# Kernel optimization log

Hardware: AMD Instinct MI355X
Metric: run time of the kernel (lower is better)

The kernel has to match this reference:

```python
import jax, jax.numpy as jnp
import numpy as np

B, S, D = 32, 512, 512
GH, LH = 8, 4            # global / local num_heads
W, STRIDE = 10, 5        # local window size and hop (window_size // 2)


def _mha(x, w_in, b_in, w_out, b_out, n_heads, key_mask=None):
    """Torch nn.MultiheadAttention (self-attn, eval mode). x: [N, L, D]."""
    N, L, d = x.shape
    dh = d // n_heads
    qkv = x @ w_in.T + b_in                       # [N, L, 3D]
    q, k, v = jnp.split(qkv, 3, axis=-1)
    def heads(t):
        return t.reshape(N, L, n_heads, dh).transpose(0, 2, 1, 3)  # [N,H,L,dh]
    q, k, v = heads(q), heads(k), heads(v)
    scores = jnp.einsum('bhqd,bhkd->bhqk', q, k) / jnp.sqrt(jnp.asarray(dh, x.dtype))
    if key_mask is not None:                      # key_mask: [N, L] bool, True = valid
        scores = jnp.where(key_mask[:, None, None, :], scores, jnp.asarray(-1e9, x.dtype))
    attn = jax.nn.softmax(scores, axis=-1)
    out = jnp.einsum('bhqk,bhkd->bhqd', attn, v).transpose(0, 2, 1, 3).reshape(N, L, d)
    return out @ w_out.T + b_out


def setup_inputs() -> dict:
    key = jax.random.key(0)
    ks = jax.random.split(key, 12)
    s = 0.02
    return {
        'x':      jax.random.normal(ks[0], (B, S, D), jnp.float32),
        'gw_in':  jax.random.normal(ks[1], (3 * D, D), jnp.float32) * s,
        'gb_in':  jnp.zeros((3 * D,), jnp.float32),
        'gw_out': jax.random.normal(ks[2], (D, D), jnp.float32) * s,
        'gb_out': jnp.zeros((D,), jnp.float32),
        'lw_in':  jax.random.normal(ks[3], (3 * D, D), jnp.float32) * s,
        'lb_in':  jnp.zeros((3 * D,), jnp.float32),
        'lw_out': jax.random.normal(ks[4], (D, D), jnp.float32) * s,
        'lb_out': jnp.zeros((D,), jnp.float32),
        'fw':     jax.random.normal(ks[5], (D, 2 * D), jnp.float32) * s,
        'fb':     jnp.zeros((D,), jnp.float32),
    }


def reference(x, gw_in, gb_in, gw_out, gb_out, lw_in, lb_in, lw_out, lb_out, fw, fb):
    # ---- global branch: full self-attention over the sequence ----
    global_out = _mha(x, gw_in, gb_in, gw_out, gb_out, GH)

    # ---- local branch: overlapping windows of size W, hop STRIDE ----
    starts = np.arange(0, S, STRIDE)              # static window starts
    NW = len(starts)
    pos = starts[:, None] + np.arange(W)          # [NW, W] absolute positions
    valid = pos < S                               # ragged tail windows
    idx = np.minimum(pos, S - 1)                  # clipped gather indices

    windows = x[:, idx]                           # [B, NW, W, D]
    windows = windows.reshape(B * NW, W, D)
    key_mask = jnp.broadcast_to(jnp.asarray(valid)[None], (B, NW, W)).reshape(B * NW, W)

    local_attn = _mha(windows, lw_in, lb_in, lw_out, lb_out, LH, key_mask=key_mask)
    local_attn = local_attn.reshape(B, NW, W, D) * jnp.asarray(valid)[None, :, :, None].astype(x.dtype)

    # scatter-add overlapping window outputs back (matches `local_out[:, i:end] +=`)
    local_out = jnp.zeros_like(x).at[:, idx.reshape(-1)].add(local_attn.reshape(B, NW * W, D))

    # ---- fusion MLP (dropout = identity in eval) ----
    combined = jnp.concatenate([global_out, local_out], axis=-1)   # [B, S, 2D]
    return jax.nn.relu(combined @ fw.T + fb)
```

## Files before the change

### kernel.cpp

```cpp
#include <hip/hip_runtime.h>
#include <cstdint>
#include <cstddef>

#define DEV __device__ __forceinline__

typedef float f32x4 __attribute__((ext_vector_type(4)));
typedef short bf16x8 __attribute__((ext_vector_type(8)));

DEV unsigned short f2bf(float f) {
  union { float f; unsigned u; } v; v.f = f;
  unsigned u = v.u;
  unsigned r = u + 0x7FFFu + ((u >> 16) & 1u);
  return (unsigned short)(r >> 16);
}
DEV float bf2f(unsigned short h) {
  union { unsigned u; float f; } v; v.u = ((unsigned)h) << 16;
  return v.f;
}
DEV unsigned cvtpk(float lo, float hi) {
  unsigned r;
  asm("v_cvt_pk_bf16_f32 %0, %1, %2" : "=v"(r) : "v"(lo), "v"(hi));
  return r;
}

DEV void gload16(const void* g, void* l) {
  __builtin_amdgcn_global_load_lds((const __attribute__((address_space(1))) unsigned int*)g,
                                   (__attribute__((address_space(3))) unsigned int*)l,
                                   16, 0, 0);
}

DEV f32x4 MFMA(bf16x8 a, bf16x8 b, f32x4 c) {
  return __builtin_amdgcn_mfma_f32_16x16x32_bf16(a, b, c, 0, 0, 0);
}

__global__ void k_f2bf(const float* __restrict__ src, unsigned short* __restrict__ dst, int n) {
  int i = (blockIdx.x * blockDim.x + threadIdx.x) * 4;
  int stride = gridDim.x * blockDim.x * 4;
  for (; i < n; i += stride) {
    float4 v = *(const float4*)(src + i);
    ushort4 o;
    o.x = f2bf(v.x); o.y = f2bf(v.y); o.z = f2bf(v.z); o.w = f2bf(v.w);
    *(ushort4*)(dst + i) = o;
  }
}

__global__ __launch_bounds__(256) void k_merge(const float* __restrict__ fw,
                                               const float* __restrict__ gw_out,
                                               const float* __restrict__ lw_out,
                                               unsigned short* __restrict__ M1b,
                                               unsigned short* __restrict__ M2b) {
  __shared__ float Fa[64][68];
  __shared__ float Gb[64][68];
  const int bi = blockIdx.x, bj = blockIdx.y, m2 = blockIdx.z;
  const float* g = m2 ? lw_out : gw_out;
  const int i0 = bi * 64, j0 = bj * 64;
  const int tid = threadIdx.x;
  const int tr = tid >> 4, tc = tid & 15;
  float acc[4][4] = {};
  for (int kc = 0; kc < 8; kc++) {
    int k0 = kc * 64;
    __syncthreads();
    #pragma unroll
    for (int it = 0; it < 4; it++) {
      int r = tr + 16 * it;
      float4 v = *(const float4*)(fw + (size_t)(i0 + r) * 1024 + m2 * 512 + k0 + tc * 4);
      Fa[tc * 4 + 0][r] = v.x; Fa[tc * 4 + 1][r] = v.y;
      Fa[tc * 4 + 2][r] = v.z; Fa[tc * 4 + 3][r] = v.w;
      *(float4*)&Gb[r][tc * 4] = *(const float4*)(g + (size_t)(k0 + r) * 512 + j0 + tc * 4);
    }
    __syncthreads();
    for (int k = 0; k < 64; k++) {
      float4 a4 = *(const float4*)&Fa[k][tr * 4];
      float4 b4 = *(const float4*)&Gb[k][tc * 4];
      float av[4] = {a4.x, a4.y, a4.z, a4.w};
      float bv[4] = {b4.x, b4.y, b4.z, b4.w};
      #pragma unroll
      for (int r = 0; r < 4; r++)
        #pragma unroll
        for (int c = 0; c < 4; c++)
          acc[r][c] += av[r] * bv[c];
    }
  }
  unsigned short* M = m2 ? M2b : M1b;
  #pragma unroll
  for (int r = 0; r < 4; r++) {
    ushort4 pk;
    pk.x = f2bf(acc[r][0]); pk.y = f2bf(acc[r][1]);
    pk.z = f2bf(acc[r][2]); pk.w = f2bf(acc[r][3]);
    *(ushort4*)&M[(size_t)(i0 + tr * 4 + r) * 512 + j0 + tc * 4] = pk;
  }
}

__global__ __launch_bounds__(256) void k_bias(const float* __restrict__ fw, const float* __restrict__ gb_out,
                                              const float* __restrict__ lb_out, const float* __restrict__ fb,
                                              float* __restrict__ bias1, float* __restrict__ bias2) {
  __shared__ float bv[512];
  const int which = blockIdx.y;
  const int i0 = blockIdx.x * 64;
  const float* src = which ? lb_out : gb_out;
  for (int t = threadIdx.x; t < 512; t += 256) bv[t] = src[t];
  __syncthreads();
  const int r = threadIdx.x >> 2, c4 = threadIdx.x & 3;
  const float* frow = fw + (size_t)(i0 + r) * 1024 + (which ? 512 : 0) + c4 * 128;
  float a = 0.f;
  #pragma unroll 4
  for (int k = 0; k < 128; k += 4) {
    float4 v = *(const float4*)(frow + k);
    a += v.x * bv[c4 * 128 + k] + v.y * bv[c4 * 128 + k + 1]
       + v.z * bv[c4 * 128 + k + 2] + v.w * bv[c4 * 128 + k + 3];
  }
  a += __shfl_xor(a, 1);
  a += __shfl_xor(a, 2);
  if (c4 == 0) {
    int i = i0 + r;
    if (which) bias2[i] = a;
    else       bias1[i] = a + fb[i];
  }
}

template <int EPI>
__global__ __launch_bounds__(256) void k_gemm(const unsigned short* __restrict__ A,
                                              const unsigned short* __restrict__ A2,
                                              const unsigned short* __restrict__ Wm,
                                              const unsigned short* __restrict__ W2,
                                              const float* __restrict__ bias,
                                              const float* __restrict__ bias2,
                                              float qscale, void* __restrict__ Cout,
                                              int Ntot, int NT) {
  __shared__ unsigned short As[2][128 * 32];
  __shared__ unsigned short Bs[2][128 * 32];
  const int tid = threadIdx.x;
  const int wave = tid >> 6, lane = tid & 63;
  const int wr = wave >> 1, wc = wave & 1;
  const int bm = blockIdx.x, bn = blockIdx.y;
  const int ql = lane & 15, kg = lane >> 4;

  const int c0 = wave * 2;
  const int srow = lane >> 2;
  const int sks = (lane & 3) * 8;

  auto stage = [&](int buf, int t) {
    const unsigned short* sA = A;
    const unsigned short* sW = Wm;
    int k0 = t * 32;
    if (EPI == 1 && t >= 16) { sA = A2; sW = W2; k0 = (t - 16) * 32; }
    #pragma unroll
    for (int i = 0; i < 2; i++) {
      int c = c0 + i;
      int row = c * 16 + srow;
      gload16(sA + (size_t)(bm * 128 + row) * 512 + k0 + sks, &As[buf][c * 512 + lane * 8]);
      gload16(sW + (size_t)(bn * 128 + row) * 512 + k0 + sks, &Bs[buf][c * 512 + lane * 8]);
    }
  };

  f32x4 acc[4][4] = {};
  stage(0, 0);
  __syncthreads();
  for (int t = 0; t < NT; t++) {
    int buf = t & 1;
    if (t + 1 < NT) stage(buf ^ 1, t + 1);
    const unsigned short* as = As[buf];
    const unsigned short* bs = Bs[buf];
    bf16x8 af[4], bfr[4];
    #pragma unroll
    for (int m = 0; m < 4; m++)
      af[m] = *(const bf16x8*)&as[(wr * 64 + m * 16 + ql) * 32 + kg * 8];
    #pragma unroll
    for (int n = 0; n < 4; n++)
      bfr[n] = *(const bf16x8*)&bs[(wc * 64 + n * 16 + ql) * 32 + kg * 8];
    #pragma unroll
    for (int m = 0; m < 4; m++)
      #pragma unroll
      for (int n = 0; n < 4; n++)
        acc[m][n] = MFMA(af[m], bfr[n], acc[m][n]);
    __syncthreads();
  }

  const int row0 = bm * 128 + wr * 64;
  const int col0 = bn * 128 + wc * 64;
  if (EPI == 0) {
    unsigned short* C = (unsigned short*)Cout;
    #pragma unroll
    for (int m = 0; m < 4; m++)
      #pragma unroll
      for (int n = 0; n < 4; n++) {
        int col = col0 + n * 16 + ql;
        float bcol = bias[col];
        float qs = (col < 512) ? qscale : 1.0f;
        #pragma unroll
        for (int r = 0; r < 4; r++) {
          int row = row0 + m * 16 + kg * 4 + r;
          C[(size_t)row * Ntot + col] = f2bf((acc[m][n][r] + bcol) * qs);
        }
      }
  } else {
    float* C = (float*)Cout;
    #pragma unroll
    for (int m = 0; m < 4; m++)
      #pragma unroll
      for (int n = 0; n < 4; n++) {
        int col = col0 + n * 16 + ql;
        float b1 = bias[col], b2 = bias2[col];
        #pragma unroll
        for (int r = 0; r < 4; r++) {
          int row = row0 + m * 16 + kg * 4 + r;
          float cc = ((row & 511) < 5) ? 1.0f : 2.0f;
          float v = acc[m][n][r] + b1 + cc * b2;
          C[(size_t)row * 512 + col] = fmaxf(v, 0.0f);
        }
      }
  }
}

__global__ __launch_bounds__(1024, 4) void k_attn_g(const unsigned short* __restrict__ QKV,
                                                    unsigned short* __restrict__ Og) {
  __shared__ unsigned short Klds[512 * 64];
  __shared__ unsigned short Vt[64 * 512];
  const int tid = threadIdx.x, wave = tid >> 6, lane = tid & 63;
  const int ql = lane & 15, kg = lane >> 4;
  const int h = blockIdx.x, b = blockIdx.y;
  const size_t tb = (size_t)b * 512;
  const size_t hoff = (size_t)h * 64;

  #pragma unroll
  for (int i = 0; i < 4; i++) {
    int instr = wave * 4 + i;
    int row = instr * 8 + (lane >> 3);
    int slot = lane & 7;
    int c = slot ^ (row & 7);
    gload16(QKV + (tb + row) * 1536 + 512 + hoff + c * 8, &Klds[instr * 512 + lane * 8]);
  }
  {
    int key = tid & 511;
    int cb = (tid >> 9) * 4;
    int k64 = key & 63;
    int f = k64 >> 4, kgv = (k64 >> 2) & 3, r = k64 & 3;
    int col = (key & ~63) + 32 * (f >> 1) + 4 * (f & 1) + 8 * kgv + r;
    const unsigned short* Vp = QKV + (tb + key) * 1536 + 1024 + hoff;
    #pragma unroll
    for (int c8 = 0; c8 < 4; c8++) {
      bf16x8 v8 = *(const bf16x8*)(Vp + (cb + c8) * 8);
      #pragma unroll
      for (int j = 0; j < 8; j++) {
        int d = (cb + c8) * 8 + j;
        Vt[d * 512 + (((col >> 3) ^ (d & 7)) * 8) + (col & 7)] = (unsigned short)v8[j];
      }
    }
  }
  bf16x8 qf[2][2];
  #pragma unroll
  for (int m = 0; m < 2; m++) {
    const unsigned short* Qp = QKV + (tb + wave * 32 + m * 16 + ql) * 1536 + hoff;
    qf[m][0] = *(const bf16x8*)(Qp + kg * 8);
    qf[m][1] = *(const bf16x8*)(Qp + 32 + kg * 8);
  }
  __syncthreads();

  float l_part[2] = {};
  f32x4 ot[2][4] = {};

  for (int kv = 0; kv < 8; kv++) {
    const int k0 = kv * 64;
    bf16x8 kf[4][2], vb[4][2];
    #pragma unroll
    for (int f = 0; f < 4; f++) {
      int row = k0 + 16 * f + ql;
      #pragma unroll
      for (int c = 0; c < 2; c++)
        kf[f][c] = *(const bf16x8*)&Klds[row * 64 + (((c * 4 + kg) ^ (row & 7)) * 8)];
      int d = 16 * f + ql;
      #pragma unroll
      for (int st = 0; st < 2; st++) {
        int cb_r = (k0 >> 3) + st * 4 + kg;
        vb[f][st] = *(const bf16x8*)&Vt[d * 512 + ((cb_r ^ (d & 7)) * 8)];
      }
    }
    #pragma unroll
    for (int m = 0; m < 2; m++) {
      f32x4 s[4] = {};
      #pragma unroll
      for (int f = 0; f < 4; f++) {
        s[f] = MFMA(kf[f][0], qf[m][0], s[f]);
        s[f] = MFMA(kf[f][1], qf[m][1], s[f]);
      }
      #pragma unroll
      for (int f = 0; f < 4; f++) {
        #pragma unroll
        for (int r = 0; r < 4; r++)
          s[f][r] = exp2f(s[f][r]);
        l_part[m] += (s[f][0] + s[f][1]) + (s[f][2] + s[f][3]);
      }
      #pragma unroll
      for (int st = 0; st < 2; st++) {
        union { unsigned w[4]; bf16x8 v; } pb;
        #pragma unroll
        for (int w = 0; w < 4; w++) {
          int f = 2 * st + (w >> 1);
          pb.w[w] = cvtpk(s[f][2 * (w & 1)], s[f][2 * (w & 1) + 1]);
        }
        #pragma unroll
        for (int fp = 0; fp < 4; fp++)
          ot[m][fp] = MFMA(vb[fp][st], pb.v, ot[m][fp]);
      }
    }
  }

  #pragma unroll
  for (int m = 0; m < 2; m++) {
    float l = l_part[m];
    l += __shfl_xor(l, 16);
    l += __shfl_xor(l, 32);
    float inv = 1.0f / l;
    size_t row = tb + wave * 32 + m * 16 + ql;
    #pragma unroll
    for (int fp = 0; fp < 4; fp++) {
      ushort4 st4;
      st4.x = f2bf(ot[m][fp][0] * inv);
      st4.y = f2bf(ot[m][fp][1] * inv);
      st4.z = f2bf(ot[m][fp][2] * inv);
      st4.w = f2bf(ot[m][fp][3] * inv);
      *(ushort4*)&Og[row * 512 + hoff + 16 * fp + 4 * kg] = st4;
    }
  }
}

__global__ __launch_bounds__(256) void k_attn_l(const unsigned short* __restrict__ QKV,
                                                unsigned short* __restrict__ Lacc) {
  __shared__ unsigned short Qs[5][520];
  __shared__ unsigned short Ks[15][520];
  __shared__ unsigned short Vs[15][520];
  __shared__ float Pb[2][4][5][13];
  const int w = blockIdx.x, b = blockIdx.y;
  const int p0 = 5 * w;
  const int tid = threadIdx.x;
  const size_t tbase = (size_t)b * 512;

  for (int c = tid; c < 35 * 64; c += 256) {
    int row = c >> 6, ch = (c & 63) * 8;
    if (row < 5) {
      int tok = min(p0 + row, 511);
      *(bf16x8*)&Qs[row][ch] = *(const bf16x8*)(QKV + (tbase + tok) * 1536 + ch);
    } else if (row < 20) {
      int rr = row - 5;
      int tok = min(max(p0 - 5 + rr, 0), 511);
      *(bf16x8*)&Ks[rr][ch] = *(const bf16x8*)(QKV + (tbase + tok) * 1536 + 512 + ch);
    } else {
      int rr = row - 20;
      int tok = min(max(p0 - 5 + rr, 0), 511);
      *(bf16x8*)&Vs[rr][ch] = *(const bf16x8*)(QKV + (tbase + tok) * 1536 + 1024 + ch);
    }
  }
  __syncthreads();

  #pragma unroll
  for (int rep = 0; rep < 2; rep++) {
    int idx = tid + rep * 256;
    if (idx < 400) {
      int j = idx % 10;
      int t1 = idx / 10;
      int q = t1 % 5;
      int t2 = t1 / 5;
      int h = t2 & 3;
      int win = t2 >> 2;
      int krow = win ? j : j + 5;
      int ktok = p0 - 5 + krow;
      float scv = -1e30f;
      bool ok = (win == 0 || w > 0) && (p0 + q < 512) && (ktok < 512);
      if (ok) {
        float acc = 0.f;
        const unsigned short* qp = &Qs[q][h * 128];
        const unsigned short* kp = &Ks[krow][h * 128];
        #pragma unroll
        for (int ck = 0; ck < 16; ck++) {
          bf16x8 q8 = *(const bf16x8*)(qp + ck * 8);
          bf16x8 k8 = *(const bf16x8*)(kp + ck * 8);
          #pragma unroll
          for (int e = 0; e < 8; e++)
            acc += bf2f((unsigned short)q8[e]) * bf2f((unsigned short)k8[e]);
        }
        scv = acc;
      }
      Pb[win][h][q][j] = scv;
    }
  }
  __syncthreads();

  if (tid < 40) {
    int q = tid % 5;
    int t2 = tid / 5;
    int h = t2 & 3;
    int win = t2 >> 2;
    float* row = &Pb[win][h][q][0];
    float mx = -1e30f;
    #pragma unroll
    for (int j = 0; j < 10; j++) mx = fmaxf(mx, row[j]);
    float e[10]; float su = 0.f;
    #pragma unroll
    for (int j = 0; j < 10; j++) {
      float v = row[j];
      float ej = (v <= -1e29f) ? 0.f : exp2f(v - mx);
      e[j] = ej; su += ej;
    }
    float inv = (su > 0.f) ? 1.0f / su : 0.f;
    #pragma unroll
    for (int j = 0; j < 10; j++) row[j] = e[j] * inv;
  }
  __syncthreads();

  {
    const int h = tid >> 6;
    const int d = tid * 2;
    for (int qq = 0; qq < 5; qq++) {
      int p = p0 + qq;
      if (p >= 512) break;
      float a0 = 0.f, a1 = 0.f;
      const float* P0 = &Pb[0][h][qq][0];
      #pragma unroll
      for (int j = 0; j < 10; j++) {
        float pw = P0[j];
        a0 += pw * bf2f(Vs[j + 5][d]);
        a1 += pw * bf2f(Vs[j + 5][d + 1]);
      }
      if (w > 0) {
        const float* P1 = &Pb[1][h][qq][0];
        #pragma unroll
        for (int j = 0; j < 10; j++) {
          float pw = P1[j];
          a0 += pw * bf2f(Vs[j][d]);
          a1 += pw * bf2f(Vs[j][d + 1]);
        }
      }
      ushort2 st; st.x = f2bf(a0); st.y = f2bf(a1);
      *(ushort2*)&Lacc[(tbase + p) * 512 + d] = st;
    }
  }
}

extern "C" void kernel_launch(void* const* d_in, const int* in_sizes, int n_in,
                              void* d_out, int out_size, void* d_ws, size_t ws_size,
                              hipStream_t stream) {
  const float* x      = (const float*)d_in[0];
  const float* gw_in  = (const float*)d_in[1];
  const float* gb_in  = (const float*)d_in[2];
  const float* gw_out = (const float*)d_in[3];
  const float* gb_out = (const float*)d_in[4];
  const float* lw_in  = (const float*)d_in[5];
  const float* lb_in  = (const float*)d_in[6];
  const float* lw_out = (const float*)d_in[7];
  const float* lb_out = (const float*)d_in[8];
  const float* fw     = (const float*)d_in[9];
  const float* fb     = (const float*)d_in[10];

  char* ws = (char*)d_ws;
  auto alloc = [&](size_t bytes) -> char* {
    char* p = ws;
    ws += (bytes + 255) & ~(size_t)255;
    return p;
  };
  unsigned short* xb     = (unsigned short*)alloc((size_t)16384 * 512 * 2);
  unsigned short* gwin_b = (unsigned short*)alloc((size_t)1536 * 512 * 2);
  unsigned short* lwin_b = (unsigned short*)alloc((size_t)1536 * 512 * 2);
  unsigned short* M1b    = (unsigned short*)alloc((size_t)512 * 512 * 2);
  unsigned short* M2b    = (unsigned short*)alloc((size_t)512 * 512 * 2);
  float* bias1           = (float*)alloc(512 * 4);
  float* bias2           = (float*)alloc(512 * 4);
  unsigned short* QKV    = (unsigned short*)alloc((size_t)16384 * 1536 * 2);
  unsigned short* Og     = (unsigned short*)alloc((size_t)16384 * 512 * 2);
  unsigned short* La     = (unsigned short*)alloc((size_t)16384 * 512 * 2);

  k_f2bf<<<2048, 256, 0, stream>>>(x, xb, 16384 * 512);
  k_f2bf<<<128, 256, 0, stream>>>(gw_in, gwin_b, 1536 * 512);
  k_f2bf<<<128, 256, 0, stream>>>(lw_in, lwin_b, 1536 * 512);
  k_merge<<<dim3(8, 8, 2), 256, 0, stream>>>(fw, gw_out, lw_out, M1b, M2b);
  k_bias<<<dim3(8, 2), 256, 0, stream>>>(fw, gb_out, lb_out, fb, bias1, bias2);

  k_gemm<0><<<dim3(128, 12), 256, 0, stream>>>(xb, nullptr, gwin_b, nullptr, gb_in, nullptr,
                                               0.125f * 1.44269504f, QKV, 1536, 16);
  k_attn_g<<<dim3(8, 32), 1024, 0, stream>>>(QKV, Og);

  k_gemm<0><<<dim3(128, 12), 256, 0, stream>>>(xb, nullptr, lwin_b, nullptr, lb_in, nullptr,
                                               0.08838834764831845f * 1.44269504f, QKV, 1536, 16);
  k_attn_l<<<dim3(103, 32), 256, 0, stream>>>(QKV, La);

  k_gemm<1><<<dim3(128, 4), 256, 0, stream>>>(Og, La, M1b, M2b, bias1, bias2,
                                              1.0f, d_out, 512, 32);
}
```

Before: 214.9 us.

## Restructure GEMM to two waves with 128x64 per-wave tiles and XOR-swizzled LDS

The bf16 GEMM now runs with 128 threads (2 waves) per 128x128 block instead of 4 waves. Each wave computes a 128x64 output tile with 8x4 MFMA accumulators, so each LDS B fragment is reused across 8 A fragments. The shared-memory staging layout gains an XOR swizzle on the k-chunk index to avoid bank conflicts on fragment reads. The aim is more MFMA work per LDS read and fewer bank conflicts. The cost is double the accumulator registers per wave and fewer waves to hide memory latency.

```diff
diff --git a/kernel.cpp b/kernel.cpp
--- a/kernel.cpp
+++ b/kernel.cpp
@@ -119,25 +119,20 @@
 }
 
 template <int EPI>
-__global__ __launch_bounds__(256) void k_gemm(const unsigned short* __restrict__ A,
-                                              const unsigned short* __restrict__ A2,
-                                              const unsigned short* __restrict__ Wm,
-                                              const unsigned short* __restrict__ W2,
-                                              const float* __restrict__ bias,
-                                              const float* __restrict__ bias2,
-                                              float qscale, void* __restrict__ Cout,
-                                              int Ntot, int NT) {
+__global__ __launch_bounds__(128) void k_gemm2(const unsigned short* __restrict__ A,
+                                               const unsigned short* __restrict__ A2,
+                                               const unsigned short* __restrict__ Wm,
+                                               const unsigned short* __restrict__ W2,
+                                               const float* __restrict__ bias,
+                                               const float* __restrict__ bias2,
+                                               float qscale, void* __restrict__ Cout,
+                                               int Ntot, int NT) {
   __shared__ unsigned short As[2][128 * 32];
   __shared__ unsigned short Bs[2][128 * 32];
   const int tid = threadIdx.x;
   const int wave = tid >> 6, lane = tid & 63;
-  const int wr = wave >> 1, wc = wave & 1;
   const int bm = blockIdx.x, bn = blockIdx.y;
   const int ql = lane & 15, kg = lane >> 4;
-
-  const int c0 = wave * 2;
-  const int srow = lane >> 2;
-  const int sks = (lane & 3) * 8;
 
   auto stage = [&](int buf, int t) {
     const unsigned short* sA = A;
@@ -145,67 +140,69 @@
     int k0 = t * 32;
     if (EPI == 1 && t >= 16) { sA = A2; sW = W2; k0 = (t - 16) * 32; }
     #pragma unroll
-    for (int i = 0; i < 2; i++) {
-      int c = c0 + i;
-      int row = c * 16 + srow;
-      gload16(sA + (size_t)(bm * 128 + row) * 512 + k0 + sks, &As[buf][c * 512 + lane * 8]);
-      gload16(sW + (size_t)(bn * 128 + row) * 512 + k0 + sks, &Bs[buf][c * 512 + lane * 8]);
+    for (int i = 0; i < 4; i++) {
+      int n = i * 128 + tid;
+      int row = n >> 2, s = n & 3;
+      int c = s ^ ((row >> 1) & 3);
+      gload16(sA + (size_t)(bm * 128 + row) * 512 + k0 + c * 8, &As[buf][n * 8]);
+      gload16(sW + (size_t)(bn * 128 + row) * 512 + k0 + c * 8, &Bs[buf][n * 8]);
     }
   };
 
-  f32x4 acc[4][4] = {};
+  const int offs = ql * 32 + ((kg ^ ((ql >> 1) & 3)) * 8);
+
+  f32x4 acc[8][4] = {};
   stage(0, 0);
   __syncthreads();
   for (int t = 0; t < NT; t++) {
     int buf = t & 1;
     if (t + 1 < NT) stage(buf ^ 1, t + 1);
     const unsigned short* as = As[buf];
-    const unsigned short* bs = Bs[buf];
-    bf16x8 af[4], bfr[4];
-    #pragma unroll
-    for (int m = 0; m < 4; m++)
-      af[m] = *(const bf16x8*)&as[(wr * 64 + m * 16 + ql) * 32 + kg * 8];
-    #pragma unroll
-    for (int n = 0; n < 4; n++)
-      bfr[n] = *(const bf16x8*)&bs[(wc * 64 + n * 16 + ql) * 32 + kg * 8];
-    #pragma unroll
-    for (int m = 0; m < 4; m++)
-      #pragma unroll
-      for (int n = 0; n < 4; n++)
-        acc[m][n] = MFMA(af[m], bfr[n], acc[m][n]);
+    const unsigned short* bs = Bs[buf] + wave * 2048;
+    bf16x8 bfr[4];
+    #pragma unroll
+    for (int nq = 0; nq < 4; nq++)
+      bfr[nq] = *(const bf16x8*)(bs + nq * 512 + offs);
+    #pragma unroll
+    for (int mq = 0; mq < 8; mq++) {
+      bf16x8 af = *(const bf16x8*)(as + mq * 512 + offs);
+      #pragma unroll
+      for (int nq = 0; nq < 4; nq++)
+        acc[mq][nq] = MFMA(af, bfr[nq], acc[mq][nq]);
+    }
     __syncthreads();
   }
 
-  const int row0 = bm * 128 + wr * 64;
-  const int col0 = bn * 128 + wc * 64;
+  const int row0 = bm * 128;
+  const int col0 = bn * 128 + wave * 64;
   if (EPI == 0) {
     unsigned short* C = (unsigned short*)Cout;
     #pragma unroll
-    for (int m = 0; m < 4; m++)
-      #pragma unroll
-      for (int n = 0; n < 4; n++) {
-        int col = col0 + n * 16 + ql;
+    for (int mq = 0; mq < 8; mq++)
+      #pragma unroll
+      for (int nq = 0; nq < 4; nq++) {
+        int col = col0 + nq * 16 + ql;
         float bcol = bias[col];
         float qs = (col < 512) ? qscale : 1.0f;
         #pragma unroll
         for (int r = 0; r < 4; r++) {
-          int row = row0 + m * 16 + kg * 4 + r;
-          C[(size_t)row * Ntot + col] = f2bf((acc[m][n][r] + bcol) * qs);
+          int row = row0 + mq * 16 + kg * 4 + r;
+          C[(size_t)row * Ntot + col] = f2bf((acc[mq][nq][r] + bcol) * qs);
         }
       }
   } else {
     float* C = (float*)Cout;
     #pragma unroll
-    for (int m = 0; m < 4; m++)
-      #pragma unroll
-      for (int n = 0; n < 4; n++) {
-        int col = col0 + n * 16 + ql;
+    for (int mq = 0; mq < 8; mq++)
+      #pragma unroll
+      for (int nq = 0; nq < 4; nq++) {
+        int col = col0 + nq * 16 + ql;
         float b1 = bias[col], b2 = bias2[col];
         #pragma unroll
         for (int r = 0; r < 4; r++) {
-          int row = row0 + m * 16 + kg * 4 + r;
+          int row = row0 + mq * 16 + kg * 4 + r;
           float cc = ((row & 511) < 5) ? 1.0f : 2.0f;
-          float v = acc[m][n][r] + b1 + cc * b2;
+          float v = acc[mq][nq][r] + b1 + cc * b2;
           C[(size_t)row * 512 + col] = fmaxf(v, 0.0f);
         }
       }
@@ -474,14 +471,14 @@
   k_merge<<<dim3(8, 8, 2), 256, 0, stream>>>(fw, gw_out, lw_out, M1b, M2b);
   k_bias<<<dim3(8, 2), 256, 0, stream>>>(fw, gb_out, lb_out, fb, bias1, bias2);
 
-  k_gemm<0><<<dim3(128, 12), 256, 0, stream>>>(xb, nullptr, gwin_b, nullptr, gb_in, nullptr,
-                                               0.125f * 1.44269504f, QKV, 1536, 16);
+  k_gemm2<0><<<dim3(128, 12), 128, 0, stream>>>(xb, nullptr, gwin_b, nullptr, gb_in, nullptr,
+                                                0.125f * 1.44269504f, QKV, 1536, 16);
   k_attn_g<<<dim3(8, 32), 1024, 0, stream>>>(QKV, Og);
 
-  k_gemm<0><<<dim3(128, 12), 256, 0, stream>>>(xb, nullptr, lwin_b, nullptr, lb_in, nullptr,
-                                               0.08838834764831845f * 1.44269504f, QKV, 1536, 16);
+  k_gemm2<0><<<dim3(128, 12), 128, 0, stream>>>(xb, nullptr, lwin_b, nullptr, lb_in, nullptr,
+                                                0.08838834764831845f * 1.44269504f, QKV, 1536, 16);
   k_attn_l<<<dim3(103, 32), 256, 0, stream>>>(QKV, La);
 
-  k_gemm<1><<<dim3(128, 4), 256, 0, stream>>>(Og, La, M1b, M2b, bias1, bias2,
-                                              1.0f, d_out, 512, 32);
-}
+  k_gemm2<1><<<dim3(128, 4), 128, 0, stream>>>(Og, La, M1b, M2b, bias1, bias2,
+                                               1.0f, d_out, 512, 32);
+}
```

New measurement: 252.5 us. 17.5% more time.
